# Performance work log

Measured on AMD Instinct MI355X. Metric: run time of the kernel, lower is better.

## Reference

```python
import jax, jax.numpy as jnp
import numpy as np


def setup_inputs() -> dict:
    key = jax.random.key(0)
    B, D, C, H = 4096, 64, 128, 512
    ks = jax.random.split(key, 6)
    return {
        "q_z_x_params": jax.random.normal(ks[0], (B, C), jnp.float32),
        "eps": jax.random.normal(ks[1], (B, D), jnp.float32),
        "W1": jax.random.normal(ks[2], (D + C, H), jnp.float32) / np.sqrt(D + C).astype(np.float32),
        "b1": jnp.zeros((H,), jnp.float32),
        "W2": jax.random.normal(ks[3], (H, H), jnp.float32) / np.sqrt(H).astype(np.float32),
        "b2": jnp.zeros((H,), jnp.float32),
        "W3": jax.random.normal(ks[4], (H, 2 * D), jnp.float32) / np.sqrt(H).astype(np.float32),
        "b3": jnp.zeros((2 * D,), jnp.float32),
    }


def _made_masks(D, C, H):
    # Standard MADE degrees, natural ordering; context columns fully connected.
    m_in = np.arange(1, D + 1)                      # input degrees 1..D
    m_h = (np.arange(H) % (D - 1)) + 1              # hidden degrees 1..D-1
    M1 = np.concatenate([m_h[None, :] >= m_in[:, None],
                         np.ones((C, H), bool)], axis=0)   # (D+C, H)
    M2 = m_h[None, :] >= m_h[:, None]               # (H, H)
    m_out = np.tile(np.arange(1, D + 1), 2)         # (2D,) mean||prescale
    M3 = m_out[None, :] > m_h[:, None]              # (H, 2D)
    f32 = jnp.float32
    return jnp.asarray(M1, f32), jnp.asarray(M2, f32), jnp.asarray(M3, f32)


def reference(q_z_x_params, eps, W1, b1, W2, b2, W3, b3):
    B, D = eps.shape
    C = q_z_x_params.shape[1]
    H = W2.shape[0]
    M1, M2, M3 = _made_masks(D, C, H)
    mW1, mW2, mW3 = W1 * M1, W2 * M2, W3 * M3

    def made(z):
        x = jnp.concatenate([z, q_z_x_params], axis=1)   # (B, D+C)
        h1 = jax.nn.relu(x @ mW1 + b1)
        h2 = jax.nn.relu(h1 @ mW2 + b2)
        out = h2 @ mW3 + b3                              # (B, 2D)
        return out[:, :D], out[:, D:]

    def step(z, i):
        mean, prescale = made(z)
        mu_i = jnp.take(mean, i, axis=1)                 # (B,)
        scale_i = jax.nn.softplus(jnp.take(prescale, i, axis=1))
        z_i = mu_i + scale_i * jnp.take(eps, i, axis=1)  # reparameterized Normal sample
        z = z.at[:, i].set(z_i)
        return z, None

    z0 = jnp.zeros((B, D), eps.dtype)
    z_sample, _ = jax.lax.scan(step, z0, jnp.arange(D))
    return z_sample
```

## Files before the change

kernel.cpp:

```cpp
#include <hip/hip_runtime.h>
#include <math.h>

#define DD 64
#define CC 128
#define HH 512
#define BATCH 4096

typedef __attribute__((ext_vector_type(2))) float f32x2;
typedef unsigned long long u64;

__device__ __forceinline__ f32x2 splat2(float x) { f32x2 v; v[0] = x; v[1] = x; return v; }

__device__ __forceinline__ f32x2 pk_fma_s(u64 hpair, f32x2 b, f32x2 c) {
    f32x2 d;
    asm("v_pk_fma_f32 %0, %1, %2, %3" : "=v"(d) : "s"(hpair), "v"(b), "v"(c));
    return d;
}

__device__ __forceinline__ float fast_softplus(float x) {
    float t = exp2f(-fabsf(x) * 1.44269504f);
    return fmaxf(x, 0.f) + 0.69314718f * log2f(1.f + t);
}

__device__ __forceinline__ float bcast(float x, int l) {
    return __int_as_float(__builtin_amdgcn_readlane(__float_as_int(x), l));
}
__device__ __forceinline__ u64 rl_pair(float x, int l) {
    unsigned u = (unsigned)__builtin_amdgcn_readlane(__float_as_int(x), l);
    return ((u64)u << 32) | u;
}

typedef const __attribute__((address_space(1))) void* as1_cptr;
typedef __attribute__((address_space(3))) void* as3_ptr;
__device__ __forceinline__ void glds16(const float* g, float* l) {
    __builtin_amdgcn_global_load_lds((as1_cptr)g, (as3_ptr)l, 16, 0, 0);
}

#define WAIT_VM(N) asm volatile("s_waitcnt vmcnt(" #N ")" ::: "memory")
#define CFENCE()   asm volatile("" ::: "memory")

__global__ __launch_bounds__(256, 2) void made_sample(
    const float* __restrict__ ctx,
    const float* __restrict__ eps,
    const float* __restrict__ W1,
    const float* __restrict__ b1,
    const float* __restrict__ W2,
    const float* __restrict__ b2,
    const float* __restrict__ W3,
    const float* __restrict__ b3,
    float* __restrict__ out)
{
    const int lane  = threadIdx.x & 63;
    const int w     = threadIdx.x >> 6;
    const int rbase = blockIdx.x * 8 + w * 2;
    const int jbase = 8 * lane;

    __shared__ float sbuf[3][10 * HH];
    __shared__ float w3sb[3][5 * 256];

    int deg[8];
    #pragma unroll
    for (int u = 0; u < 8; ++u) deg[u] = (jbase + u) % 63 + 1;

    auto load8v = [&](const float* base_, f32x2* r_) {
        float4 a = *(const float4*)(base_ + lane * 4);
        float4 b = *(const float4*)(base_ + 256 + lane * 4);
        r_[0][0] = a.x; r_[0][1] = a.y; r_[1][0] = a.z; r_[1][1] = a.w;
        r_[2][0] = b.x; r_[2][1] = b.y; r_[3][0] = b.z; r_[3][1] = b.w;
    };
    auto stage_row = [&](const float* src, float* dst) {
        glds16(src + lane * 8,     dst);
        glds16(src + lane * 8 + 4, dst + 256);
    };
    auto stage_w3pair = [&](int k0, int k1, float* dst) {
        const float* g = (lane < 32) ? (W3 + k0 * (2 * DD) + lane * 4)
                                     : (W3 + k1 * (2 * DD) + (lane - 32) * 4);
        glds16(g, dst);
    };

    f32x2 p1[2][4], p2[2][4];
    #pragma unroll
    for (int j = 0; j < 4; ++j) {
        f32x2 t1, t2;
        t1[0] = b1[jbase + 2 * j]; t1[1] = b1[jbase + 2 * j + 1];
        t2[0] = b2[jbase + 2 * j]; t2[1] = b2[jbase + 2 * j + 1];
        p1[0][j] = t1; p1[1][j] = t1;
        p2[0][j] = t2; p2[1][j] = t2;
    }
    f32x2 accA[2], accB[2];
    accA[0] = splat2(0.f); accA[1] = splat2(0.f);
    accB[0] = splat2(0.f); accB[1] = splat2(0.f);

    float ca[2], cb[2], ep[2];
    #pragma unroll
    for (int r = 0; r < 2; ++r) {
        ca[r] = ctx[(rbase + r) * CC + lane];
        cb[r] = ctx[(rbase + r) * CC + 64 + lane];
        ep[r] = eps[(rbase + r) * DD + lane];
    }
    const float b3m = b3[lane];
    const float b3p = b3[64 + lane];

    auto stage_ctx = [&](int ch, float* buf) {
        stage_row(W1 + (DD + 8 * ch + 2 * w) * HH,     buf + (2 * w) * HH);
        stage_row(W1 + (DD + 8 * ch + 2 * w + 1) * HH, buf + (2 * w + 1) * HH);
    };
    auto stage_step = [&](int in, float* buf, float* w3buf) {
        const int basen = (in == 0) ? 0 : (in - 1);
        const int r8 = (basen + 504 < HH) ? (basen + 504) : (HH - 1);
        stage_row(W2 + (basen + 63 * w) * HH,       buf + w * HH);
        stage_row(W2 + (basen + 63 * (4 + w)) * HH, buf + (4 + w) * HH);
        if (w == 0) stage_row(W2 + r8 * HH, buf + 8 * HH);
        if (w == 1) stage_row(W1 + in * HH, buf + 9 * HH);
        stage_w3pair(basen + 63 * (2 * w), basen + 63 * (2 * w + 1),
                     w3buf + w * 256);
        if (w == 2) stage_w3pair(r8, r8, w3buf + 4 * 256);
    };
    auto wait_step = [&]() {
        if (w == 0 || w == 1) WAIT_VM(7);
        else if (w == 2)      WAIT_VM(6);
        else                  WAIT_VM(5);
    };

    stage_ctx(0, sbuf[0]);
    stage_ctx(1, sbuf[1]);
    int bc = 0;
    #pragma unroll 1
    for (int ch = 0; ch < 16; ++ch) {
        if (ch < 15) WAIT_VM(4); else WAIT_VM(0);
        __builtin_amdgcn_s_barrier();
        CFENCE();
        __builtin_amdgcn_sched_barrier(0);
        const int b2i = (bc < 1) ? bc + 2 : bc - 1;
        if (ch < 14) stage_ctx(ch + 2, sbuf[b2i]);
        float* cur = sbuf[bc];
        #pragma unroll
        for (int q = 0; q < 8; ++q) {
            f32x2 cw[4];
            load8v(cur + q * HH, cw);
            const int c = 8 * ch + q;
            #pragma unroll
            for (int r = 0; r < 2; ++r) {
                const u64 cvp = rl_pair((ch < 8) ? ca[r] : cb[r], c & 63);
                #pragma unroll
                for (int j = 0; j < 4; ++j) p1[r][j] = pk_fma_s(cvp, cw[j], p1[r][j]);
            }
        }
        bc = (bc < 2) ? bc + 1 : 0;
    }
    __syncthreads();

    float z[2] = {0.f, 0.f};
    stage_step(0, sbuf[0], w3sb[0]);
    stage_step(1, sbuf[1], w3sb[1]);
    bc = 0;

    #pragma unroll 1
    for (int i = 0; i < DD; ++i) {
        if (i < 63) wait_step(); else WAIT_VM(0);
        __builtin_amdgcn_s_barrier();
        CFENCE();
        __builtin_amdgcn_sched_barrier(0);

        float* cur = sbuf[bc];
        const float* w3s = w3sb[bc];
        const int b2i = (bc < 1) ? bc + 2 : bc - 1;
        if (i < 62) stage_step(i + 2, sbuf[b2i], w3sb[b2i]);

        if (i > 0) {
            const int base = i - 1;
            const bool h9 = base < 8;

            float m[2];
            #pragma unroll
            for (int r = 0; r < 2; ++r) {
                float s[8];
                #pragma unroll
                for (int u = 0; u < 8; ++u)
                    s[u] = (deg[u] == i) ? p1[r][u >> 1][u & 1] : 0.f;
                const float sv = ((s[0] + s[1]) + (s[2] + s[3]))
                               + ((s[4] + s[5]) + (s[6] + s[7]));
                m[r] = fmaxf(sv, 0.f);
            }

            #pragma unroll
            for (int t = 0; t < 8; ++t) {
                const int k = base + 63 * t;
                f32x2 wv[4];
                load8v(cur + t * HH, wv);
                const u64 h0 = rl_pair(m[0], k >> 3);
                const u64 h1 = rl_pair(m[1], k >> 3);
                #pragma unroll
                for (int j = 0; j < 4; ++j) {
                    p2[0][j] = pk_fma_s(h0, wv[j], p2[0][j]);
                    p2[1][j] = pk_fma_s(h1, wv[j], p2[1][j]);
                }
            }
            if (h9) {
                f32x2 wv[4];
                load8v(cur + 8 * HH, wv);
                const u64 h0 = rl_pair(m[0], 63);
                const u64 h1 = rl_pair(m[1], 63);
                #pragma unroll
                for (int j = 0; j < 4; ++j) {
                    p2[0][j] = pk_fma_s(h0, wv[j], p2[0][j]);
                    p2[1][j] = pk_fma_s(h1, wv[j], p2[1][j]);
                }
            }

            float g[2];
            #pragma unroll
            for (int r = 0; r < 2; ++r) {
                float s[8];
                #pragma unroll
                for (int u = 0; u < 8; ++u)
                    s[u] = (deg[u] == i) ? p2[r][u >> 1][u & 1] : 0.f;
                const float sv = ((s[0] + s[1]) + (s[2] + s[3]))
                               + ((s[4] + s[5]) + (s[6] + s[7]));
                g[r] = fmaxf(sv, 0.f);
            }

            #pragma unroll
            for (int t = 0; t < 8; ++t) {
                const int k = base + 63 * t;
                f32x2 w3v;
                w3v[0] = w3s[t * 128 + lane];
                w3v[1] = w3s[t * 128 + 64 + lane];
                const u64 h0 = rl_pair(g[0], k >> 3);
                const u64 h1 = rl_pair(g[1], k >> 3);
                if (t & 1) {
                    accB[0] = pk_fma_s(h0, w3v, accB[0]);
                    accB[1] = pk_fma_s(h1, w3v, accB[1]);
                } else {
                    accA[0] = pk_fma_s(h0, w3v, accA[0]);
                    accA[1] = pk_fma_s(h1, w3v, accA[1]);
                }
            }
            if (h9) {
                f32x2 w3v;
                w3v[0] = w3s[8 * 128 + lane];
                w3v[1] = w3s[8 * 128 + 64 + lane];
                const u64 h0 = rl_pair(g[0], 63);
                const u64 h1 = rl_pair(g[1], 63);
                accB[0] = pk_fma_s(h0, w3v, accB[0]);
                accB[1] = pk_fma_s(h1, w3v, accB[1]);
            }
        }

        {
            f32x2 w1v[4];
            load8v(cur + 9 * HH, w1v);
            #pragma unroll
            for (int r = 0; r < 2; ++r) {
                const f32x2 at = accA[r] + accB[r];
                const float am = at[0] + b3m;
                const float ap = at[1] + b3p;
                const float sp = fast_softplus(ap);
                const float zc = fmaf(sp, ep[r], am);
                const float zi = bcast(zc, i);
                if (lane == i) z[r] = zi;
                const u64 zp = rl_pair(zc, i);
                #pragma unroll
                for (int j = 0; j < 4; ++j) p1[r][j] = pk_fma_s(zp, w1v[j], p1[r][j]);
            }
        }

        bc = (bc < 2) ? bc + 1 : 0;
    }

    #pragma unroll
    for (int r = 0; r < 2; ++r) out[(rbase + r) * DD + lane] = z[r];
}

extern "C" void kernel_launch(void* const* d_in, const int* in_sizes, int n_in,
                              void* d_out, int out_size, void* d_ws, size_t ws_size,
                              hipStream_t stream) {
    const float* ctx = (const float*)d_in[0];
    const float* eps = (const float*)d_in[1];
    const float* W1  = (const float*)d_in[2];
    const float* b1  = (const float*)d_in[3];
    const float* W2  = (const float*)d_in[4];
    const float* b2  = (const float*)d_in[5];
    const float* W3  = (const float*)d_in[6];
    const float* b3  = (const float*)d_in[7];
    (void)d_ws; (void)ws_size; (void)in_sizes; (void)n_in; (void)out_size;

    made_sample<<<BATCH / 8, 256, 0, stream>>>(ctx, eps, W1, b1, W2, b2, W3, b3,
                                               (float*)d_out);
}
```

Measured before the change: 185.2 us.

## Split hidden units across waves with all 8 rows per wave, exchanging activations via LDS

New measurement: 262.4 us. 41.7% more time.

```diff
diff --git a/kernel.cpp b/kernel.cpp
--- a/kernel.cpp
+++ b/kernel.cpp
@@ -22,9 +22,6 @@
     return fmaxf(x, 0.f) + 0.69314718f * log2f(1.f + t);
 }
 
-__device__ __forceinline__ float bcast(float x, int l) {
-    return __int_as_float(__builtin_amdgcn_readlane(__float_as_int(x), l));
-}
 __device__ __forceinline__ u64 rl_pair(float x, int l) {
     unsigned u = (unsigned)__builtin_amdgcn_readlane(__float_as_int(x), l);
     return ((u64)u << 32) | u;
@@ -37,6 +34,7 @@
 }
 
 #define WAIT_VM(N) asm volatile("s_waitcnt vmcnt(" #N ")" ::: "memory")
+#define LGKM0()    asm volatile("s_waitcnt lgkmcnt(0)" ::: "memory")
 #define CFENCE()   asm volatile("" ::: "memory")
 
 __global__ __launch_bounds__(256, 2) void made_sample(
@@ -50,27 +48,24 @@
     const float* __restrict__ b3,
     float* __restrict__ out)
 {
-    const int lane  = threadIdx.x & 63;
-    const int w     = threadIdx.x >> 6;
-    const int rbase = blockIdx.x * 8 + w * 2;
-    const int jbase = 8 * lane;
+    const int lane = threadIdx.x & 63;
+    const int w    = threadIdx.x >> 6;
+    const int blk8 = blockIdx.x * 8;
+    const int u0   = 128 * w + 2 * lane;
+    const int deg0 = (u0 % 63) + 1;
+    const int deg1 = ((u0 + 1) % 63) + 1;
+    const int t0   = u0 / 63;
+    const int t1   = (u0 + 1) / 63;
 
     __shared__ float sbuf[3][10 * HH];
     __shared__ float w3sb[3][5 * 256];
-
-    int deg[8];
-    #pragma unroll
-    for (int u = 0; u < 8; ++u) deg[u] = (jbase + u) % 63 + 1;
-
-    auto load8v = [&](const float* base_, f32x2* r_) {
-        float4 a = *(const float4*)(base_ + lane * 4);
-        float4 b = *(const float4*)(base_ + 256 + lane * 4);
-        r_[0][0] = a.x; r_[0][1] = a.y; r_[1][0] = a.z; r_[1][1] = a.w;
-        r_[2][0] = b.x; r_[2][1] = b.y; r_[3][0] = b.z; r_[3][1] = b.w;
-    };
+    __shared__ float h1t[128];
+    __shared__ float h2t[128];
+    __shared__ float zt[8];
+
     auto stage_row = [&](const float* src, float* dst) {
-        glds16(src + lane * 8,     dst);
-        glds16(src + lane * 8 + 4, dst + 256);
+        glds16(src + lane * 4,       dst);
+        glds16(src + 256 + lane * 4, dst + 256);
     };
     auto stage_w3pair = [&](int k0, int k1, float* dst) {
         const float* g = (lane < 32) ? (W3 + k0 * (2 * DD) + lane * 4)
@@ -78,26 +73,25 @@
         glds16(g, dst);
     };
 
-    f32x2 p1[2][4], p2[2][4];
-    #pragma unroll
-    for (int j = 0; j < 4; ++j) {
-        f32x2 t1, t2;
-        t1[0] = b1[jbase + 2 * j]; t1[1] = b1[jbase + 2 * j + 1];
-        t2[0] = b2[jbase + 2 * j]; t2[1] = b2[jbase + 2 * j + 1];
-        p1[0][j] = t1; p1[1][j] = t1;
-        p2[0][j] = t2; p2[1][j] = t2;
-    }
+    f32x2 p1[8], p2[8];
+    const f32x2 b1v = *(const f32x2*)(b1 + u0);
+    const f32x2 b2v = *(const f32x2*)(b2 + u0);
+    #pragma unroll
+    for (int r = 0; r < 8; ++r) { p1[r] = b1v; p2[r] = b2v; }
+
     f32x2 accA[2], accB[2];
     accA[0] = splat2(0.f); accA[1] = splat2(0.f);
     accB[0] = splat2(0.f); accB[1] = splat2(0.f);
 
-    float ca[2], cb[2], ep[2];
-    #pragma unroll
-    for (int r = 0; r < 2; ++r) {
-        ca[r] = ctx[(rbase + r) * CC + lane];
-        cb[r] = ctx[(rbase + r) * CC + 64 + lane];
-        ep[r] = eps[(rbase + r) * DD + lane];
+    float ca[8], cb[8];
+    #pragma unroll
+    for (int r = 0; r < 8; ++r) {
+        ca[r] = ctx[(blk8 + r) * CC + lane];
+        cb[r] = ctx[(blk8 + r) * CC + 64 + lane];
     }
+    float ep[2];
+    #pragma unroll
+    for (int rr = 0; rr < 2; ++rr) ep[rr] = eps[(blk8 + 2 * w + rr) * DD + lane];
     const float b3m = b3[lane];
     const float b3p = b3[64 + lane];
 
@@ -136,28 +130,28 @@
         float* cur = sbuf[bc];
         #pragma unroll
         for (int q = 0; q < 8; ++q) {
-            f32x2 cw[4];
-            load8v(cur + q * HH, cw);
+            const f32x2 wv = *(const f32x2*)(cur + q * HH + u0);
             const int c = 8 * ch + q;
             #pragma unroll
-            for (int r = 0; r < 2; ++r) {
-                const u64 cvp = rl_pair((ch < 8) ? ca[r] : cb[r], c & 63);
-                #pragma unroll
-                for (int j = 0; j < 4; ++j) p1[r][j] = pk_fma_s(cvp, cw[j], p1[r][j]);
+            for (int r = 0; r < 8; ++r) {
+                const u64 cv = rl_pair((ch < 8) ? ca[r] : cb[r], c & 63);
+                p1[r] = pk_fma_s(cv, wv, p1[r]);
             }
         }
         bc = (bc < 2) ? bc + 1 : 0;
     }
     __syncthreads();
 
-    float z[2] = {0.f, 0.f};
+    float zk[2] = {0.f, 0.f};
     stage_step(0, sbuf[0], w3sb[0]);
     stage_step(1, sbuf[1], w3sb[1]);
     bc = 0;
+    f32x2 w1v = splat2(0.f);
 
     #pragma unroll 1
     for (int i = 0; i < DD; ++i) {
         if (i < 63) wait_step(); else WAIT_VM(0);
+        LGKM0();
         __builtin_amdgcn_s_barrier();
         CFENCE();
         __builtin_amdgcn_sched_barrier(0);
@@ -167,109 +161,104 @@
         const int b2i = (bc < 1) ? bc + 2 : bc - 1;
         if (i < 62) stage_step(i + 2, sbuf[b2i], w3sb[b2i]);
 
+        const bool h9 = (i >= 1) && (i - 1 < 8);
+
         if (i > 0) {
-            const int base = i - 1;
-            const bool h9 = base < 8;
-
-            float m[2];
-            #pragma unroll
-            for (int r = 0; r < 2; ++r) {
-                float s[8];
-                #pragma unroll
-                for (int u = 0; u < 8; ++u)
-                    s[u] = (deg[u] == i) ? p1[r][u >> 1][u & 1] : 0.f;
-                const float sv = ((s[0] + s[1]) + (s[2] + s[3]))
-                               + ((s[4] + s[5]) + (s[6] + s[7]));
-                m[r] = fmaxf(sv, 0.f);
-            }
-
+            const float zv = zt[lane & 7];
+            #pragma unroll
+            for (int r = 0; r < 8; ++r) {
+                const u64 zp = rl_pair(zv, r);
+                p1[r] = pk_fma_s(zp, w1v, p1[r]);
+            }
+            if (deg0 == i) {
+                #pragma unroll
+                for (int r = 0; r < 8; ++r) h1t[t0 * 8 + r] = fmaxf(p1[r][0], 0.f);
+            }
+            if (deg1 == i) {
+                #pragma unroll
+                for (int r = 0; r < 8; ++r) h1t[t1 * 8 + r] = fmaxf(p1[r][1], 0.f);
+            }
+        }
+        LGKM0();
+        __builtin_amdgcn_s_barrier();
+        CFENCE();
+
+        w1v = *(const f32x2*)(cur + 9 * HH + u0);
+        if (i > 0) {
+            const float hv0 = h1t[lane];
+            const float hv1 = h1t[64 + lane];
             #pragma unroll
             for (int t = 0; t < 8; ++t) {
-                const int k = base + 63 * t;
-                f32x2 wv[4];
-                load8v(cur + t * HH, wv);
-                const u64 h0 = rl_pair(m[0], k >> 3);
-                const u64 h1 = rl_pair(m[1], k >> 3);
-                #pragma unroll
-                for (int j = 0; j < 4; ++j) {
-                    p2[0][j] = pk_fma_s(h0, wv[j], p2[0][j]);
-                    p2[1][j] = pk_fma_s(h1, wv[j], p2[1][j]);
+                const f32x2 wv = *(const f32x2*)(cur + t * HH + u0);
+                #pragma unroll
+                for (int r = 0; r < 8; ++r) {
+                    const u64 hp = rl_pair(hv0, t * 8 + r);
+                    p2[r] = pk_fma_s(hp, wv, p2[r]);
                 }
             }
             if (h9) {
-                f32x2 wv[4];
-                load8v(cur + 8 * HH, wv);
-                const u64 h0 = rl_pair(m[0], 63);
-                const u64 h1 = rl_pair(m[1], 63);
-                #pragma unroll
-                for (int j = 0; j < 4; ++j) {
-                    p2[0][j] = pk_fma_s(h0, wv[j], p2[0][j]);
-                    p2[1][j] = pk_fma_s(h1, wv[j], p2[1][j]);
+                const f32x2 wv = *(const f32x2*)(cur + 8 * HH + u0);
+                #pragma unroll
+                for (int r = 0; r < 8; ++r) {
+                    const u64 hp = rl_pair(hv1, r);
+                    p2[r] = pk_fma_s(hp, wv, p2[r]);
                 }
             }
-
-            float g[2];
-            #pragma unroll
-            for (int r = 0; r < 2; ++r) {
-                float s[8];
-                #pragma unroll
-                for (int u = 0; u < 8; ++u)
-                    s[u] = (deg[u] == i) ? p2[r][u >> 1][u & 1] : 0.f;
-                const float sv = ((s[0] + s[1]) + (s[2] + s[3]))
-                               + ((s[4] + s[5]) + (s[6] + s[7]));
-                g[r] = fmaxf(sv, 0.f);
-            }
-
+            if (deg0 == i) {
+                #pragma unroll
+                for (int r = 0; r < 8; ++r) h2t[t0 * 8 + r] = fmaxf(p2[r][0], 0.f);
+            }
+            if (deg1 == i) {
+                #pragma unroll
+                for (int r = 0; r < 8; ++r) h2t[t1 * 8 + r] = fmaxf(p2[r][1], 0.f);
+            }
+        }
+        LGKM0();
+        __builtin_amdgcn_s_barrier();
+        CFENCE();
+
+        if (i > 0) {
+            const float gv0 = h2t[lane];
+            const float gv1 = h2t[64 + lane];
+            const int row0 = 2 * w, row1 = 2 * w + 1;
             #pragma unroll
             for (int t = 0; t < 8; ++t) {
-                const int k = base + 63 * t;
                 f32x2 w3v;
                 w3v[0] = w3s[t * 128 + lane];
                 w3v[1] = w3s[t * 128 + 64 + lane];
-                const u64 h0 = rl_pair(g[0], k >> 3);
-                const u64 h1 = rl_pair(g[1], k >> 3);
-                if (t & 1) {
-                    accB[0] = pk_fma_s(h0, w3v, accB[0]);
-                    accB[1] = pk_fma_s(h1, w3v, accB[1]);
-                } else {
-                    accA[0] = pk_fma_s(h0, w3v, accA[0]);
-                    accA[1] = pk_fma_s(h1, w3v, accA[1]);
-                }
+                const u64 g0 = rl_pair(gv0, t * 8 + row0);
+                const u64 g1 = rl_pair(gv0, t * 8 + row1);
+                if (t & 1) { accB[0] = pk_fma_s(g0, w3v, accB[0]);
+                             accB[1] = pk_fma_s(g1, w3v, accB[1]); }
+                else       { accA[0] = pk_fma_s(g0, w3v, accA[0]);
+                             accA[1] = pk_fma_s(g1, w3v, accA[1]); }
             }
             if (h9) {
                 f32x2 w3v;
                 w3v[0] = w3s[8 * 128 + lane];
                 w3v[1] = w3s[8 * 128 + 64 + lane];
-                const u64 h0 = rl_pair(g[0], 63);
-                const u64 h1 = rl_pair(g[1], 63);
-                accB[0] = pk_fma_s(h0, w3v, accB[0]);
-                accB[1] = pk_fma_s(h1, w3v, accB[1]);
-            }
-        }
-
-        {
-            f32x2 w1v[4];
-            load8v(cur + 9 * HH, w1v);
-            #pragma unroll
-            for (int r = 0; r < 2; ++r) {
-                const f32x2 at = accA[r] + accB[r];
-                const float am = at[0] + b3m;
-                const float ap = at[1] + b3p;
-                const float sp = fast_softplus(ap);
-                const float zc = fmaf(sp, ep[r], am);
-                const float zi = bcast(zc, i);
-                if (lane == i) z[r] = zi;
-                const u64 zp = rl_pair(zc, i);
-                #pragma unroll
-                for (int j = 0; j < 4; ++j) p1[r][j] = pk_fma_s(zp, w1v[j], p1[r][j]);
-            }
+                const u64 g0 = rl_pair(gv1, row0);
+                const u64 g1 = rl_pair(gv1, row1);
+                accB[0] = pk_fma_s(g0, w3v, accB[0]);
+                accB[1] = pk_fma_s(g1, w3v, accB[1]);
+            }
+        }
+        #pragma unroll
+        for (int rr = 0; rr < 2; ++rr) {
+            const f32x2 at = accA[rr] + accB[rr];
+            const float am = at[0] + b3m;
+            const float ap = at[1] + b3p;
+            const float sp = fast_softplus(ap);
+            const float zc = fmaf(sp, ep[rr], am);
+            if (lane == i) { zk[rr] = zc; zt[2 * w + rr] = zc; }
         }
 
         bc = (bc < 2) ? bc + 1 : 0;
     }
 
     #pragma unroll
-    for (int r = 0; r < 2; ++r) out[(rbase + r) * DD + lane] = z[r];
+    for (int rr = 0; rr < 2; ++rr)
+        out[(blk8 + 2 * w + rr) * DD + lane] = zk[rr];
 }
 
 extern "C" void kernel_launch(void* const* d_in, const int* in_sizes, int n_in,
```
